# Optimization experiments

Hardware: AMD Instinct MI355X
Metric: run time of the kernel (lower is better)

Reference implementation:

```python
import jax, jax.numpy as jnp
import numpy as np

N_NODES = 50000


def gcn_conv(x, src, dst, inv_sqrt_deg, W):
    # GCNConv: h = x @ W^T, then out[i] = sum_{j->i} norm_ji * h[j]
    h = x @ W.T                                   # [N, out]
    norm = inv_sqrt_deg[src] * inv_sqrt_deg[dst]  # [E]
    msg = h[src] * norm[:, None]                  # [E, out] gather
    return jax.ops.segment_sum(msg, dst, num_segments=N_NODES)  # scatter-add


def setup_inputs() -> dict:
    key = jax.random.key(0)
    k1, k2, k3, k4, k5 = jax.random.split(key, 5)
    x = jax.random.normal(k1, (N_NODES, 500), dtype=jnp.float32)
    edge_index = jax.random.randint(k2, (2, 1600000), 0, N_NODES, dtype=jnp.int64)
    W1 = jax.random.normal(k3, (128, 500), dtype=jnp.float32) * 0.04
    W2 = jax.random.normal(k4, (128, 128), dtype=jnp.float32) * 0.08
    Wlin = jax.random.normal(k5, (16, 128), dtype=jnp.float32) * 0.08
    return {"x": x, "edge_index": edge_index, "W1": W1, "W2": W2, "Wlin": Wlin}


def reference(x, edge_index, W1, W2, Wlin):
    # add self-loops (GCNConv default)
    loop = jnp.arange(N_NODES, dtype=edge_index.dtype)
    src = jnp.concatenate([edge_index[0], loop])
    dst = jnp.concatenate([edge_index[1], loop])
    # symmetric normalization: deg counted on destination (in-degree incl. self-loop)
    deg = jax.ops.segment_sum(jnp.ones_like(src, dtype=x.dtype), dst, num_segments=N_NODES)
    inv_sqrt_deg = jnp.where(deg > 0, jax.lax.rsqrt(deg), 0.0)

    h = gcn_conv(x, src, dst, inv_sqrt_deg, W1)
    h = jax.nn.relu(h)
    h = gcn_conv(h, src, dst, inv_sqrt_deg, W2)
    # dropout is identity in eval mode (training=False reference)
    return h @ Wlin.T  # [N, num_classes]
```

## Files before the change

kernel.cpp:

```cpp
#include <hip/hip_runtime.h>

#define N_NODES 50000
#define F_IN 500
#define F_HID 128
#define F_OUT 16
#define NSCAN_BLKS ((N_NODES + 255) / 256)


__device__ __forceinline__ unsigned bf16_pack2(float a, float b) {
    unsigned ua = __float_as_uint(a);
    unsigned ub = __float_as_uint(b);
    ua = (ua + 0x7fffu + ((ua >> 16) & 1u)) >> 16;
    ub = (ub + 0x7fffu + ((ub >> 16) & 1u)) >> 16;
    return ua | (ub << 16);
}
__device__ __forceinline__ float bf_lo(unsigned v) { return __uint_as_float(v << 16); }
__device__ __forceinline__ float bf_hi(unsigned v) { return __uint_as_float(v & 0xffff0000u); }

__device__ __forceinline__ unsigned bf16_rtne(float a) {
    unsigned u = __float_as_uint(a);
    return (u + 0x7fffu + ((u >> 16) & 1u)) >> 16;
}


__global__ void k_hist_rank(const int* __restrict__ dst, int* __restrict__ hist,
                            int* __restrict__ rank, int E) {
    int e = blockIdx.x * 256 + threadIdx.x;
    if (e < E) rank[e] = atomicAdd(&hist[dst[e]], 1);
}

__global__ __launch_bounds__(256) void k_scan_local(const int* __restrict__ hist,
                                                    int* __restrict__ rowptr,
                                                    int* __restrict__ blksum) {
    __shared__ int s[256];
    const int tid = threadIdx.x;
    const int i = blockIdx.x * 256 + tid;
    int v = (i < N_NODES) ? hist[i] : 0;
    s[tid] = v;
    __syncthreads();
#pragma unroll
    for (int ofs = 1; ofs < 256; ofs <<= 1) {
        int t = (tid >= ofs) ? s[tid - ofs] : 0;
        __syncthreads();
        if (tid >= ofs) s[tid] += t;
        __syncthreads();
    }
    if (i < N_NODES) rowptr[i] = s[tid] - v;
    if (tid == 255) blksum[blockIdx.x] = s[255];
}

__global__ __launch_bounds__(256) void k_scan_blk(int* __restrict__ blksum) {
    __shared__ int s[256];
    const int tid = threadIdx.x;
    int v = (tid < NSCAN_BLKS) ? blksum[tid] : 0;
    s[tid] = v;
    __syncthreads();
#pragma unroll
    for (int ofs = 1; ofs < 256; ofs <<= 1) {
        int t = (tid >= ofs) ? s[tid - ofs] : 0;
        __syncthreads();
        if (tid >= ofs) s[tid] += t;
        __syncthreads();
    }
    if (tid < NSCAN_BLKS) blksum[tid] = s[tid] - v;
}

__global__ void k_finalize(const int* __restrict__ hist, int* __restrict__ rowptr,
                           const int* __restrict__ blksum, float* __restrict__ isd, int E) {
    int i = blockIdx.x * 256 + threadIdx.x;
    if (i < N_NODES) {
        rowptr[i] = rowptr[i] + blksum[i >> 8];
        isd[i] = rsqrtf((float)(hist[i] + 1));
    }
    if (i == 0) rowptr[N_NODES] = E;
}

__global__ void k_reorder(const int* __restrict__ src, const int* __restrict__ dst,
                          const int* __restrict__ rank, const int* __restrict__ rowptr,
                          int* __restrict__ csr_src, int E) {
    int e = blockIdx.x * 256 + threadIdx.x;
    if (e >= E) return;
    csr_src[rowptr[dst[e]] + rank[e]] = src[e];
}


__global__ void k_wc(const float* __restrict__ W2, const float* __restrict__ Wlin,
                     float* __restrict__ Wc) {
    const int c = blockIdx.x;
    const int j = threadIdx.x;
    const float* wl = Wlin + c * 128;
    float acc = 0.f;
#pragma unroll 4
    for (int k = 0; k < 128; ++k) acc += wl[k] * W2[k * 128 + j];
    Wc[c * 128 + j] = acc;
}


__global__ __launch_bounds__(256) void k_w1pack(const float* __restrict__ W1,
                                                ushort* __restrict__ wpk) {
    int t = blockIdx.x * 256 + threadIdx.x;
    if (t >= 8192) return;
    const int lane = t & 63;
    const int fkt = t >> 6;
    const int f = fkt & 7;
    const int kt = fkt >> 3;
    const int n = (f << 4) + (lane & 15);
    const int kb = (kt << 5) + ((lane >> 4) << 3);
    ushort h8[8], l8[8];
#pragma unroll
    for (int j = 0; j < 8; ++j) {
        const int k = kb + j;
        float v = (k < F_IN) ? W1[n * F_IN + k] : 0.f;
        unsigned h = bf16_rtne(v);
        float fh = __uint_as_float(h << 16);
        unsigned l = bf16_rtne(v - fh);
        h8[j] = (ushort)h;
        l8[j] = (ushort)l;
    }
    const size_t base = ((size_t)fkt << 10);
    *(uint4*)(wpk + base + (lane << 3))       = *(const uint4*)h8;
    *(uint4*)(wpk + base + 512 + (lane << 3)) = *(const uint4*)l8;
}


typedef __attribute__((ext_vector_type(8))) short s16x8;
typedef __attribute__((ext_vector_type(4))) float f32x4;

typedef const __attribute__((address_space(1))) unsigned u32_glb;
typedef __attribute__((address_space(3))) unsigned u32_lds;

__device__ __forceinline__ void glds16(const void* g, void* l) {
    __builtin_amdgcn_global_load_lds((u32_glb*)g, (u32_lds*)l, 16, 0, 0);
}

__global__ __launch_bounds__(256) void gemm1_mfma4(const float* __restrict__ A,
                                                   const ushort* __restrict__ wpk,
                                                   unsigned* __restrict__ hb, int M) {
    __shared__ __align__(16) ushort Bs[2][8192];

    const int tid = threadIdx.x;
    const int lane = tid & 63;
    const int wave = tid >> 6;
    const int jcol = lane & 15;
    const int kgrp = lane >> 4;
    const int klo  = kgrp << 3;

    const int m0  = blockIdx.x * 64 + wave * 16;
    const int arw = m0 + jcol;
    const float* arow = A + (size_t)((arw < M) ? arw : (M - 1)) * F_IN;

#define ISSUE_TILE(KT, B)                                                        \
    {                                                                            \
        const ushort* tb_ = wpk + ((size_t)(KT) << 13);                          \
        _Pragma("unroll") for (int c_ = 0; c_ < 4; ++c_) {                       \
            glds16(tb_ + ((c_ * 256 + wave * 64 + lane) << 3),                   \
                   &Bs[B][(c_ * 256 + wave * 64) << 3]);                         \
        }                                                                        \
    }

    const float4 zf4 = make_float4(0.f, 0.f, 0.f, 0.f);
    float4 ca0 = zf4, ca1 = zf4;

    ISSUE_TILE(0, 0);
    ca0 = *(const float4*)(arow + klo);
    ca1 = *(const float4*)(arow + klo + 4);
    __syncthreads();

    f32x4 acc[8] = {};

    for (int kt = 0; kt < 16; ++kt) {
        const int cb = kt & 1, nb = (kt + 1) & 1;

        float4 na0 = zf4, na1 = zf4;
        if (kt + 1 < 16) {
            ISSUE_TILE(kt + 1, nb);
            const int k = ((kt + 1) << 5) + klo;
            if (k + 8 <= F_IN) {
                na0 = *(const float4*)(arow + k);
                na1 = *(const float4*)(arow + k + 4);
            } else {
                float tmp[8];
#pragma unroll
                for (int i = 0; i < 8; ++i) tmp[i] = (k + i < F_IN) ? arow[k + i] : 0.f;
                na0 = make_float4(tmp[0], tmp[1], tmp[2], tmp[3]);
                na1 = make_float4(tmp[4], tmp[5], tmp[6], tmp[7]);
            }
        }

        const float av[8] = {ca0.x, ca0.y, ca0.z, ca0.w, ca1.x, ca1.y, ca1.z, ca1.w};
        s16x8 ahi, alo;
#pragma unroll
        for (int i = 0; i < 8; ++i) {
            unsigned h = bf16_rtne(av[i]);
            float fh = __uint_as_float(h << 16);
            unsigned l = bf16_rtne(av[i] - fh);
            ahi[i] = (short)h;
            alo[i] = (short)l;
        }

#pragma unroll
        for (int f = 0; f < 8; ++f) {
            const s16x8 bh = *(const s16x8*)&Bs[cb][(f << 10) + (lane << 3)];
            const s16x8 bl = *(const s16x8*)&Bs[cb][(f << 10) + 512 + (lane << 3)];
            acc[f] = __builtin_amdgcn_mfma_f32_16x16x32_bf16(ahi, bh, acc[f], 0, 0, 0);
            acc[f] = __builtin_amdgcn_mfma_f32_16x16x32_bf16(alo, bh, acc[f], 0, 0, 0);
            acc[f] = __builtin_amdgcn_mfma_f32_16x16x32_bf16(ahi, bl, acc[f], 0, 0, 0);
        }

        ca0 = na0;
        ca1 = na1;
        __syncthreads();
    }
#undef ISSUE_TILE

    const int orow = m0 + (kgrp << 2);
#pragma unroll
    for (int f = 0; f < 8; ++f) {
#pragma unroll
        for (int r = 0; r < 4; ++r) {
            float v = acc[f][r];
            float o = __shfl_xor(v, 1, 64);
            if (!(jcol & 1)) {
                const int m = orow + r;
                if (m < M)
                    hb[(size_t)m * 64 + (f << 3) + (jcol >> 1)] = bf16_pack2(v, o);
            }
        }
    }
}


__device__ __forceinline__ void gather_range(const unsigned* __restrict__ hh,
                                             const int* __restrict__ csr_src,
                                             const float* __restrict__ isd,
                                             float si, int lane, int e, int end,
                                             float& accx, float& accy) {
    int s[8], t[8];
    bool have = (e + 8 <= end);
    if (have) {
#pragma unroll
        for (int i = 0; i < 8; ++i) s[i] = csr_src[e + i];
    }
    while (have) {
        unsigned v[8];
        float w[8];
#pragma unroll
        for (int i = 0; i < 8; ++i) v[i] = hh[(size_t)s[i] * 64 + lane];
#pragma unroll
        for (int i = 0; i < 8; ++i) w[i] = isd[s[i]];
        const int ne = e + 8;
        const bool nhave = (ne + 8 <= end);
        if (nhave) {
#pragma unroll
            for (int i = 0; i < 8; ++i) t[i] = csr_src[ne + i];
        }
#pragma unroll
        for (int i = 0; i < 8; ++i) {
            const float wi = w[i] * si;
            accx += wi * bf_lo(v[i]);
            accy += wi * bf_hi(v[i]);
        }
#pragma unroll
        for (int i = 0; i < 8; ++i) s[i] = t[i];
        e = ne;
        have = nhave;
    }
    for (; e < end; ++e) {
        const int ss = csr_src[e];
        const float wi = isd[ss] * si;
        const unsigned v = hh[(size_t)ss * 64 + lane];
        accx += wi * bf_lo(v);
        accy += wi * bf_hi(v);
    }
}

__global__ __launch_bounds__(256) void k_gather_fused2(const unsigned* __restrict__ hh,
                                                       const int* __restrict__ rowptr,
                                                       const int* __restrict__ csr_src,
                                                       const float* __restrict__ isd,
                                                       const float* __restrict__ Wc,
                                                       float* __restrict__ z) {
    __shared__ float2 part[2][64];
    const int tid = threadIdx.x;
    const int lane = tid & 63;
    const int waveid = tid >> 6;
    const int slot = waveid >> 1;
    const int half = waveid & 1;
    const int node = (blockIdx.x << 1) + slot;

    const float si = isd[node];
    const int e0 = rowptr[node], e1 = rowptr[node + 1];
    const int mid = e0 + ((e1 - e0) >> 1);

    float accx = 0.f, accy = 0.f;
    if (half == 0) {
        const unsigned a = hh[(size_t)node * 64 + lane];
        accx = bf_lo(a) * si * si;
        accy = bf_hi(a) * si * si;
        gather_range(hh, csr_src, isd, si, lane, e0, mid, accx, accy);
    } else {
        gather_range(hh, csr_src, isd, si, lane, mid, e1, accx, accy);
        part[slot][lane] = make_float2(accx, accy);
    }
    __syncthreads();
    if (half == 1) return;

    const float2 pb = part[slot][lane];
    accx += pb.x;
    accy += pb.y;

    const float rx = fmaxf(accx, 0.f), ry = fmaxf(accy, 0.f);
    float p[16];
#pragma unroll
    for (int c = 0; c < 16; ++c) {
        const float2 wc = *(const float2*)(Wc + c * 128 + (lane << 1));
        p[c] = rx * wc.x + ry * wc.y;
    }
#pragma unroll
    for (int m = 1; m < 64; m <<= 1) {
#pragma unroll
        for (int c = 0; c < 16; ++c) p[c] += __shfl_xor(p[c], m, 64);
    }
    if (lane == 0) {
        float* zr = z + (size_t)node * 16;
        *(float4*)(zr + 0)  = make_float4(p[0],  p[1],  p[2],  p[3]);
        *(float4*)(zr + 4)  = make_float4(p[4],  p[5],  p[6],  p[7]);
        *(float4*)(zr + 8)  = make_float4(p[8],  p[9],  p[10], p[11]);
        *(float4*)(zr + 12) = make_float4(p[12], p[13], p[14], p[15]);
    }
}


__global__ __launch_bounds__(256) void k_gather16(const float4* __restrict__ z4,
                                                  const int* __restrict__ rowptr,
                                                  const int* __restrict__ csr_src,
                                                  const float* __restrict__ isd,
                                                  float4* __restrict__ out4) {
    int t = blockIdx.x * 256 + threadIdx.x;
    int n = t >> 2, q = t & 3;
    if (n >= N_NODES) return;
    const float si = isd[n];
    float4 a = z4[(size_t)n * 4 + q];
    float4 acc;
    acc.x = a.x * si * si; acc.y = a.y * si * si;
    acc.z = a.z * si * si; acc.w = a.w * si * si;
    int e = rowptr[n];
    const int end = rowptr[n + 1];
    for (; e + 4 <= end; e += 4) {
        int s0 = csr_src[e],     s1 = csr_src[e + 1];
        int s2 = csr_src[e + 2], s3 = csr_src[e + 3];
        float w0 = isd[s0] * si, w1 = isd[s1] * si;
        float w2 = isd[s2] * si, w3 = isd[s3] * si;
        float4 v0 = z4[(size_t)s0 * 4 + q];
        float4 v1 = z4[(size_t)s1 * 4 + q];
        float4 v2 = z4[(size_t)s2 * 4 + q];
        float4 v3 = z4[(size_t)s3 * 4 + q];
        acc.x += w0 * v0.x; acc.y += w0 * v0.y; acc.z += w0 * v0.z; acc.w += w0 * v0.w;
        acc.x += w1 * v1.x; acc.y += w1 * v1.y; acc.z += w1 * v1.z; acc.w += w1 * v1.w;
        acc.x += w2 * v2.x; acc.y += w2 * v2.y; acc.z += w2 * v2.z; acc.w += w2 * v2.w;
        acc.x += w3 * v3.x; acc.y += w3 * v3.y; acc.z += w3 * v3.z; acc.w += w3 * v3.w;
    }
    for (; e < end; ++e) {
        int s = csr_src[e];
        float w = isd[s] * si;
        float4 v = z4[(size_t)s * 4 + q];
        acc.x += w * v.x; acc.y += w * v.y; acc.z += w * v.z; acc.w += w * v.w;
    }
    out4[(size_t)n * 4 + q] = acc;
}


__global__ void k_deg_init(float* __restrict__ deg) {
    int i = blockIdx.x * 256 + threadIdx.x;
    if (i < N_NODES) deg[i] = 1.0f;
}
__global__ void k_deg_count(const int* __restrict__ dst, float* __restrict__ deg, int E) {
    int e = blockIdx.x * 256 + threadIdx.x;
    if (e < E) atomicAdd(&deg[dst[e]], 1.0f);
}
__global__ void k_rsqrt(float* __restrict__ deg) {
    int i = blockIdx.x * 256 + threadIdx.x;
    if (i < N_NODES) deg[i] = rsqrtf(deg[i]);
}
__global__ void k_agg_init(const float4* __restrict__ h, const float* __restrict__ isd,
                           float4* __restrict__ agg) {
    int t = blockIdx.x * 256 + threadIdx.x;
    if (t < N_NODES * (F_HID / 4)) {
        int row = t >> 5;
        float s = isd[row];
        s = s * s;
        float4 v = h[t];
        v.x *= s; v.y *= s; v.z *= s; v.w *= s;
        agg[t] = v;
    }
}
__global__ void k_scatter(const float4* __restrict__ h, const int* __restrict__ src,
                          const int* __restrict__ dst, const float* __restrict__ isd,
                          float* __restrict__ agg, int E) {
    int t = blockIdx.x * 256 + threadIdx.x;
    int e = t >> 5, q = t & 31;
    if (e >= E) return;
    int s = src[e], d = dst[e];
    float norm = isd[s] * isd[d];
    float4 v = h[(long long)s * 32 + q];
    float* out = agg + (long long)d * F_HID + q * 4;
    atomicAdd(out + 0, v.x * norm);
    atomicAdd(out + 1, v.y * norm);
    atomicAdd(out + 2, v.z * norm);
    atomicAdd(out + 3, v.w * norm);
}
template <int BM, int BN, int BK, int TM, int TN, bool RELU_A>
__global__ __launch_bounds__(256) void gemm_nt(const float* __restrict__ A,
                                               const float* __restrict__ B,
                                               float* __restrict__ C,
                                               int M, int N, int K) {
    __shared__ float As[BK][BM + 1];
    __shared__ float Bs[BK][BN + 1];
    const int tid = threadIdx.x;
    const int NTX = BN / TN;
    const int tx = tid % NTX;
    const int ty = tid / NTX;
    const int m0 = blockIdx.x * BM;
    const int n0 = blockIdx.y * BN;
    float acc[TM][TN] = {};
    for (int k0 = 0; k0 < K; k0 += BK) {
        for (int idx = tid; idx < BM * BK; idx += 256) {
            int m = idx / BK, k = idx % BK;
            int gm = m0 + m;
            float v = (gm < M) ? A[(long long)gm * K + k0 + k] : 0.0f;
            if (RELU_A) v = fmaxf(v, 0.0f);
            As[k][m] = v;
        }
        for (int idx = tid; idx < BN * BK; idx += 256) {
            int n = idx / BK, k = idx % BK;
            int gn = n0 + n;
            Bs[k][n] = (gn < N) ? B[(long long)gn * K + k0 + k] : 0.0f;
        }
        __syncthreads();
        for (int k = 0; k < BK; ++k) {
            float a[TM], b[TN];
#pragma unroll
            for (int r = 0; r < TM; ++r) a[r] = As[k][ty * TM + r];
#pragma unroll
            for (int c = 0; c < TN; ++c) b[c] = Bs[k][c * NTX + tx];
#pragma unroll
            for (int r = 0; r < TM; ++r)
#pragma unroll
                for (int c = 0; c < TN; ++c) acc[r][c] += a[r] * b[c];
        }
        __syncthreads();
    }
#pragma unroll
    for (int r = 0; r < TM; ++r) {
        int gm = m0 + ty * TM + r;
        if (gm >= M) continue;
#pragma unroll
        for (int c = 0; c < TN; ++c) {
            int gn = n0 + c * NTX + tx;
            if (gn < N) C[(long long)gm * N + gn] = acc[r][c];
        }
    }
}
__global__ __launch_bounds__(256) void gemm_lin(const float* __restrict__ A,
                                                const float* __restrict__ W,
                                                float* __restrict__ C, int M) {
    __shared__ float Ws[16][129];
    __shared__ float As[16][129];
    const int tid = threadIdx.x;
    for (int idx = tid; idx < 16 * 128; idx += 256) Ws[idx >> 7][idx & 127] = W[idx];
    const int m0 = blockIdx.x * 16;
    for (int idx = tid; idx < 16 * 128; idx += 256) {
        int r = idx >> 7, k = idx & 127;
        int gm = m0 + r;
        As[r][k] = (gm < M) ? A[(long long)gm * 128 + k] : 0.0f;
    }
    __syncthreads();
    const int tc = tid & 15, tr = tid >> 4;
    float s = 0.f;
#pragma unroll 8
    for (int k = 0; k < 128; ++k) s += As[tr][k] * Ws[tc][k];
    int gm = m0 + tr;
    if (gm < M) C[gm * 16 + tc] = s;
}


static inline size_t align256(size_t x) { return (x + 255) & ~(size_t)255; }

extern "C" void kernel_launch(void* const* d_in, const int* in_sizes, int n_in,
                              void* d_out, int out_size, void* d_ws, size_t ws_size,
                              hipStream_t stream) {
    const float* x    = (const float*)d_in[0];
    const int*   ei   = (const int*)d_in[1];
    const float* W1   = (const float*)d_in[2];
    const float* W2   = (const float*)d_in[3];
    const float* Wlin = (const float*)d_in[4];
    float* out = (float*)d_out;

    const int E = in_sizes[1] / 2;
    const int* src = ei;
    const int* dst = ei + E;

    char* ws = (char*)d_ws;
    size_t off = 0;
    float* isd  = (float*)(ws + off); off += align256((size_t)N_NODES * 4);
    float* Wc   = (float*)(ws + off); off += align256(16 * 128 * 4);
    float* bufA = (float*)(ws + off); off += align256((size_t)N_NODES * F_HID * 4);
    float* bufB = (float*)(ws + off); off += align256((size_t)N_NODES * F_HID * 4);
    int*   hist    = (int*)(ws + off); off += align256((size_t)N_NODES * 4);
    int*   rowptr  = (int*)(ws + off); off += align256(((size_t)N_NODES + 1) * 4);
    int*   blksum  = (int*)(ws + off); off += align256(256 * 4);
    int*   csr_src = (int*)(ws + off); off += align256((size_t)E * 4);
    int*   rank    = (int*)(ws + off); off += align256((size_t)E * 4);
    ushort* wpk    = (ushort*)(ws + off); off += align256((size_t)16 * 8192 * 2);
    const bool use_csr = (off <= ws_size);

    const int nblk_nodes = NSCAN_BLKS;
    const int nblk_edges = (E + 255) / 256;
    const int mtiles = (N_NODES + 63) / 64;

    if (use_csr) {
        unsigned* hb = (unsigned*)bufB;
        float*    z  = bufA;

        hipMemsetAsync(hist, 0, (size_t)N_NODES * 4, stream);
        k_hist_rank<<<nblk_edges, 256, 0, stream>>>(dst, hist, rank, E);
        k_scan_local<<<nblk_nodes, 256, 0, stream>>>(hist, rowptr, blksum);
        k_scan_blk<<<1, 256, 0, stream>>>(blksum);
        k_finalize<<<nblk_nodes, 256, 0, stream>>>(hist, rowptr, blksum, isd, E);
        k_reorder<<<nblk_edges, 256, 0, stream>>>(src, dst, rank, rowptr, csr_src, E);
        k_wc<<<16, 128, 0, stream>>>(W2, Wlin, Wc);
        k_w1pack<<<32, 256, 0, stream>>>(W1, wpk);
        gemm1_mfma4<<<mtiles, 256, 0, stream>>>(x, wpk, hb, N_NODES);
        k_gather_fused2<<<N_NODES / 2, 256, 0, stream>>>(
            hb, rowptr, csr_src, isd, Wc, z);
        k_gather16<<<(N_NODES * 4 + 255) / 256, 256, 0, stream>>>(
            (const float4*)z, rowptr, csr_src, isd, (float4*)out);
    } else {
        const int nblk_feat = (N_NODES * (F_HID / 4) + 255) / 256;
        const int nblk_scatter = (int)(((long long)E * 32 + 255) / 256);
        k_deg_init<<<(N_NODES + 255) / 256, 256, 0, stream>>>(isd);
        k_deg_count<<<nblk_edges, 256, 0, stream>>>(dst, isd, E);
        k_rsqrt<<<(N_NODES + 255) / 256, 256, 0, stream>>>(isd);
        gemm_nt<64, 128, 20, 4, 8, false>
            <<<dim3(mtiles, 1), 256, 0, stream>>>(x, W1, bufA, N_NODES, F_HID, F_IN);
        k_agg_init<<<nblk_feat, 256, 0, stream>>>((const float4*)bufA, isd, (float4*)bufB);
        k_scatter<<<nblk_scatter, 256, 0, stream>>>((const float4*)bufA, src, dst, isd, bufB, E);
        gemm_nt<64, 128, 16, 4, 8, true>
            <<<dim3(mtiles, 1), 256, 0, stream>>>(bufB, W2, bufA, N_NODES, F_HID, F_HID);
        k_agg_init<<<nblk_feat, 256, 0, stream>>>((const float4*)bufA, isd, (float4*)bufB);
        k_scatter<<<nblk_scatter, 256, 0, stream>>>((const float4*)bufA, src, dst, isd, bufB, E);
        gemm_lin<<<(N_NODES + 15) / 16, 256, 0, stream>>>(bufB, Wlin, out, N_NODES);
    }
}
```

Before: 437.0 us.

## Fold source-side degree normalization into producers to drop per-edge isd gathers

The symmetric normalization is factored so the source-side 1/sqrt(deg) is applied once per node. It is applied in the GEMM1 epilogue for layer 1 and in the z output of the fused gather for layer 2, and the destination-side factor is applied after accumulation. This removes the per-edge random isd loads and multiplies from both gather kernels, so the inner loops only load neighbor rows and add. The layer-1 tail loop is also rewritten as a clamped, predicated batch of 8 loads so the leftover edges are fetched in parallel. In exchange the GEMM epilogue gains a few loads, and pre-scaling before the bf16 rounding slightly shifts numerics.

```diff
diff --git a/kernel.cpp b/kernel.cpp
--- a/kernel.cpp
+++ b/kernel.cpp
@@ -133,8 +133,9 @@
     __builtin_amdgcn_global_load_lds((u32_glb*)g, (u32_lds*)l, 16, 0, 0);
 }
 
-__global__ __launch_bounds__(256) void gemm1_mfma4(const float* __restrict__ A,
+__global__ __launch_bounds__(256) void gemm1_mfma5(const float* __restrict__ A,
                                                    const ushort* __restrict__ wpk,
+                                                   const float* __restrict__ isd,
                                                    unsigned* __restrict__ hb, int M) {
     __shared__ __align__(16) ushort Bs[2][8192];
 
@@ -214,11 +215,17 @@
 #undef ISSUE_TILE
 
     const int orow = m0 + (kgrp << 2);
+    float sr[4];
+#pragma unroll
+    for (int r = 0; r < 4; ++r) {
+        const int m = orow + r;
+        sr[r] = (m < M) ? isd[m] : 0.f;
+    }
 #pragma unroll
     for (int f = 0; f < 8; ++f) {
 #pragma unroll
         for (int r = 0; r < 4; ++r) {
-            float v = acc[f][r];
+            float v = acc[f][r] * sr[r];
             float o = __shfl_xor(v, 1, 64);
             if (!(jcol & 1)) {
                 const int m = orow + r;
@@ -232,8 +239,7 @@
 
 __device__ __forceinline__ void gather_range(const unsigned* __restrict__ hh,
                                              const int* __restrict__ csr_src,
-                                             const float* __restrict__ isd,
-                                             float si, int lane, int e, int end,
+                                             int lane, int e, int end,
                                              float& accx, float& accy) {
     int s[8], t[8];
     bool have = (e + 8 <= end);
@@ -243,11 +249,8 @@
     }
     while (have) {
         unsigned v[8];
-        float w[8];
 #pragma unroll
         for (int i = 0; i < 8; ++i) v[i] = hh[(size_t)s[i] * 64 + lane];
-#pragma unroll
-        for (int i = 0; i < 8; ++i) w[i] = isd[s[i]];
         const int ne = e + 8;
         const bool nhave = (ne + 8 <= end);
         if (nhave) {
@@ -256,21 +259,29 @@
         }
 #pragma unroll
         for (int i = 0; i < 8; ++i) {
-            const float wi = w[i] * si;
-            accx += wi * bf_lo(v[i]);
-            accy += wi * bf_hi(v[i]);
+            accx += bf_lo(v[i]);
+            accy += bf_hi(v[i]);
         }
 #pragma unroll
         for (int i = 0; i < 8; ++i) s[i] = t[i];
         e = ne;
         have = nhave;
     }
-    for (; e < end; ++e) {
-        const int ss = csr_src[e];
-        const float wi = isd[ss] * si;
-        const unsigned v = hh[(size_t)ss * 64 + lane];
-        accx += wi * bf_lo(v);
-        accy += wi * bf_hi(v);
+    if (e < end) {
+        const int last = end - 1;
+        int ss[8];
+        unsigned vv[8];
+#pragma unroll
+        for (int i = 0; i < 8; ++i) ss[i] = csr_src[(e + i < end) ? e + i : last];
+#pragma unroll
+        for (int i = 0; i < 8; ++i) vv[i] = hh[(size_t)ss[i] * 64 + lane];
+#pragma unroll
+        for (int i = 0; i < 8; ++i) {
+            if (e + i < end) {
+                accx += bf_lo(vv[i]);
+                accy += bf_hi(vv[i]);
+            }
+        }
     }
 }
 
@@ -288,18 +299,17 @@
     const int half = waveid & 1;
     const int node = (blockIdx.x << 1) + slot;
 
-    const float si = isd[node];
     const int e0 = rowptr[node], e1 = rowptr[node + 1];
     const int mid = e0 + ((e1 - e0) >> 1);
 
     float accx = 0.f, accy = 0.f;
     if (half == 0) {
         const unsigned a = hh[(size_t)node * 64 + lane];
-        accx = bf_lo(a) * si * si;
-        accy = bf_hi(a) * si * si;
-        gather_range(hh, csr_src, isd, si, lane, e0, mid, accx, accy);
+        accx = bf_lo(a);
+        accy = bf_hi(a);
+        gather_range(hh, csr_src, lane, e0, mid, accx, accy);
     } else {
-        gather_range(hh, csr_src, isd, si, lane, mid, e1, accx, accy);
+        gather_range(hh, csr_src, lane, mid, e1, accx, accy);
         part[slot][lane] = make_float2(accx, accy);
     }
     __syncthreads();
@@ -309,7 +319,8 @@
     accx += pb.x;
     accy += pb.y;
 
-    const float rx = fmaxf(accx, 0.f), ry = fmaxf(accy, 0.f);
+    const float si = isd[node];
+    const float rx = fmaxf(accx * si, 0.f), ry = fmaxf(accy * si, 0.f);
     float p[16];
 #pragma unroll
     for (int c = 0; c < 16; ++c) {
@@ -323,10 +334,10 @@
     }
     if (lane == 0) {
         float* zr = z + (size_t)node * 16;
-        *(float4*)(zr + 0)  = make_float4(p[0],  p[1],  p[2],  p[3]);
-        *(float4*)(zr + 4)  = make_float4(p[4],  p[5],  p[6],  p[7]);
-        *(float4*)(zr + 8)  = make_float4(p[8],  p[9],  p[10], p[11]);
-        *(float4*)(zr + 12) = make_float4(p[12], p[13], p[14], p[15]);
+        *(float4*)(zr + 0)  = make_float4(si * p[0],  si * p[1],  si * p[2],  si * p[3]);
+        *(float4*)(zr + 4)  = make_float4(si * p[4],  si * p[5],  si * p[6],  si * p[7]);
+        *(float4*)(zr + 8)  = make_float4(si * p[8],  si * p[9],  si * p[10], si * p[11]);
+        *(float4*)(zr + 12) = make_float4(si * p[12], si * p[13], si * p[14], si * p[15]);
     }
 }
 
@@ -340,32 +351,27 @@
     int n = t >> 2, q = t & 3;
     if (n >= N_NODES) return;
     const float si = isd[n];
-    float4 a = z4[(size_t)n * 4 + q];
-    float4 acc;
-    acc.x = a.x * si * si; acc.y = a.y * si * si;
-    acc.z = a.z * si * si; acc.w = a.w * si * si;
+    float4 acc = z4[(size_t)n * 4 + q];
     int e = rowptr[n];
     const int end = rowptr[n + 1];
     for (; e + 4 <= end; e += 4) {
         int s0 = csr_src[e],     s1 = csr_src[e + 1];
         int s2 = csr_src[e + 2], s3 = csr_src[e + 3];
-        float w0 = isd[s0] * si, w1 = isd[s1] * si;
-        float w2 = isd[s2] * si, w3 = isd[s3] * si;
         float4 v0 = z4[(size_t)s0 * 4 + q];
         float4 v1 = z4[(size_t)s1 * 4 + q];
         float4 v2 = z4[(size_t)s2 * 4 + q];
         float4 v3 = z4[(size_t)s3 * 4 + q];
-        acc.x += w0 * v0.x; acc.y += w0 * v0.y; acc.z += w0 * v0.z; acc.w += w0 * v0.w;
-        acc.x += w1 * v1.x; acc.y += w1 * v1.y; acc.z += w1 * v1.z; acc.w += w1 * v1.w;
-        acc.x += w2 * v2.x; acc.y += w2 * v2.y; acc.z += w2 * v2.z; acc.w += w2 * v2.w;
-        acc.x += w3 * v3.x; acc.y += w3 * v3.y; acc.z += w3 * v3.z; acc.w += w3 * v3.w;
+        acc.x += v0.x + v1.x + v2.x + v3.x;
+        acc.y += v0.y + v1.y + v2.y + v3.y;
+        acc.z += v0.z + v1.z + v2.z + v3.z;
+        acc.w += v0.w + v1.w + v2.w + v3.w;
     }
     for (; e < end; ++e) {
         int s = csr_src[e];
-        float w = isd[s] * si;
         float4 v = z4[(size_t)s * 4 + q];
-        acc.x += w * v.x; acc.y += w * v.y; acc.z += w * v.z; acc.w += w * v.w;
-    }
+        acc.x += v.x; acc.y += v.y; acc.z += v.z; acc.w += v.w;
+    }
+    acc.x *= si; acc.y *= si; acc.z *= si; acc.w *= si;
     out4[(size_t)n * 4 + q] = acc;
 }
 
@@ -530,7 +536,7 @@
         k_reorder<<<nblk_edges, 256, 0, stream>>>(src, dst, rank, rowptr, csr_src, E);
         k_wc<<<16, 128, 0, stream>>>(W2, Wlin, Wc);
         k_w1pack<<<32, 256, 0, stream>>>(W1, wpk);
-        gemm1_mfma4<<<mtiles, 256, 0, stream>>>(x, wpk, hb, N_NODES);
+        gemm1_mfma5<<<mtiles, 256, 0, stream>>>(x, wpk, isd, hb, N_NODES);
         k_gather_fused2<<<N_NODES / 2, 256, 0, stream>>>(
             hb, rowptr, csr_src, isd, Wc, z);
         k_gather16<<<(N_NODES * 4 + 255) / 256, 256, 0, stream>>>(
```

After: 405.1 us. 1.08x faster.
